# Kernel tuning notes

Measured on AMD Instinct MI355X. Metric: run time of the kernel, lower is better.

The kernel has to match this reference:

```python
import math
import jax, jax.numpy as jnp
import numpy as np

EPS = 1e-5  # BatchNorm2d default eps


def setup_inputs() -> dict:
    key = jax.random.key(0)
    ks = jax.random.split(key, 12)
    C, I = 256, 128  # in_channels, inter_channels (= C // reduction)
    n, h, w = 4, 64, 64
    s = 0.02
    return {
        "x": jax.random.normal(ks[0], (n, C, h, w), jnp.float32),
        "g_w": jax.random.normal(ks[1], (I, C), jnp.float32) * s,
        "g_b": jax.random.normal(ks[2], (I,), jnp.float32) * s,
        "theta_w": jax.random.normal(ks[3], (I, C), jnp.float32) * s,
        "theta_b": jax.random.normal(ks[4], (I,), jnp.float32) * s,
        "phi_w": jax.random.normal(ks[5], (I, C), jnp.float32) * s,
        "phi_b": jax.random.normal(ks[6], (I,), jnp.float32) * s,
        "out_w": jax.random.normal(ks[7], (C, I), jnp.float32) * s,
        "bn_gamma": jax.random.uniform(ks[8], (C,), jnp.float32, 0.5, 1.5),
        "bn_beta": jax.random.normal(ks[9], (C,), jnp.float32) * s,
        "bn_mean": jax.random.normal(ks[10], (C,), jnp.float32) * s,
        "bn_var": jax.random.uniform(ks[11], (C,), jnp.float32, 0.5, 1.5),
    }


def reference(x, g_w, g_b, theta_w, theta_b, phi_w, phi_b, out_w,
              bn_gamma, bn_beta, bn_mean, bn_var):
    n, c, h, w = x.shape
    xf = x.reshape(n, c, h * w)  # (n, C, N)

    def proj(Wm, b):  # 1x1 conv == per-position linear: (n, I, N)
        return jnp.einsum('ic,ncp->nip', Wm, xf) + b[None, :, None]

    g_x = proj(g_w, g_b)          # (n, I, N)
    theta_x = proj(theta_w, theta_b)  # (n, I, N)
    phi_x = proj(phi_w, phi_b)        # (n, I, N)

    # dot_product mode: softmax FIRST, then divide by sqrt(C) (faithful to source)
    scores = jnp.einsum('nip,niq->npq', theta_x, phi_x)  # (n, N, N)
    attn = jax.nn.softmax(scores, axis=-1) / math.sqrt(c)

    y = jnp.einsum('npq,niq->nip', attn, g_x)  # (n, I, N)
    y = y.reshape(n, -1, h, w)                 # (n, I, h, w)

    # conv_out: 1x1 conv (no bias) + BatchNorm2d (eval-mode running stats)
    y = jnp.einsum('oi,nihw->nohw', out_w, y)  # (n, C, h, w)
    inv = bn_gamma / jnp.sqrt(bn_var + EPS)
    y = y * inv[None, :, None, None] + (bn_beta - bn_mean * inv)[None, :, None, None]
    return y + x
```

## Files before the change

kernel.cpp:

```cpp
#include <hip/hip_runtime.h>

typedef short short8 __attribute__((ext_vector_type(8)));
typedef short short4v __attribute__((ext_vector_type(4)));
typedef float f32x4 __attribute__((ext_vector_type(4)));
typedef float f32x16 __attribute__((ext_vector_type(16)));
typedef unsigned int uint4v __attribute__((ext_vector_type(4)));
typedef unsigned int uint2v __attribute__((ext_vector_type(2)));

#define NB 4
#define CD 256
#define ID 128
#define NP 4096

static __device__ __forceinline__ short f2bf(float f){
  unsigned u = __float_as_uint(f);
  u += 0x7FFF + ((u >> 16) & 1);
  return (short)(u >> 16);
}
static __device__ __forceinline__ float bf2f(short s){
  unsigned u = ((unsigned)(unsigned short)s) << 16;
  return __uint_as_float(u);
}
static __device__ __forceinline__ unsigned cvtpk(float lo, float hi){
  unsigned r;
  asm("v_cvt_pk_bf16_f32 %0, %1, %2" : "=v"(r) : "v"(lo), "v"(hi));
  return r;
}
static __device__ __forceinline__ float fexp2(float x){
  float r;
  asm("v_exp_f32 %0, %1" : "=v"(r) : "v"(x));
  return r;
}
static __device__ __forceinline__ unsigned pack4_fp8(float a, float b, float c, float d){
  unsigned lo, hi;
  asm("v_cvt_pk_fp8_f32 %0, %1, %2" : "=v"(lo) : "v"(a), "v"(b));
  asm("v_cvt_pk_fp8_f32 %0, %1, %2" : "=v"(hi) : "v"(c), "v"(d));
  return (lo & 0xffffu) | (hi << 16);
}
static __device__ __forceinline__ unsigned char f2fp8(float v){
  unsigned u;
  asm("v_cvt_pk_fp8_f32 %0, %1, %1" : "=v"(u) : "v"(v));
  return (unsigned char)u;
}

static __device__ __forceinline__ void gload16(const void* g, void* l){
  __builtin_amdgcn_global_load_lds(
      (const __attribute__((address_space(1))) unsigned int*)g,
      (__attribute__((address_space(3))) unsigned int*)l, 16, 0, 0);
}

__global__ __launch_bounds__(256) void k_cvtw(const float* __restrict__ g_w,
    const float* __restrict__ th_w, const float* __restrict__ ph_w,
    const float* __restrict__ out_w, short* __restrict__ wb){
  int idx = (blockIdx.x * 256 + threadIdx.x) * 4;
  const float* s;
  int sel = idx >> 15;
  if(sel == 0) s = g_w; else if(sel == 1) s = th_w; else if(sel == 2) s = ph_w; else s = out_w;
  int off = idx & 32767;
  float4 v = *reinterpret_cast<const float4*>(s + off);
  short4v o = { f2bf(v.x), f2bf(v.y), f2bf(v.z), f2bf(v.w) };
  *reinterpret_cast<short4v*>(wb + idx) = o;
}

__global__ __launch_bounds__(512) void k_proj(const float* __restrict__ x,
    const short* __restrict__ wb, const float* __restrict__ g_b,
    const float* __restrict__ th_b, const float* __restrict__ ph_b,
    unsigned char* __restrict__ q8, unsigned char* __restrict__ k8,
    unsigned char* __restrict__ v8){
  __shared__ __align__(16) char smem[98304];
  char* XT = smem + 65536;
  int b = blockIdx.x;
  int n = b >> 6, pt = b & 63;
  int pb0 = pt * 64;
  int t = threadIdx.x, w = t >> 6, l = t & 63;
  int lr = l & 15, lg = l >> 4;
  int i0 = w * 16;

  const char* xg = (const char*)(x + ((size_t)n * CD) * NP + pb0);
#pragma unroll
  for(int i_ = 0; i_ < 8; ++i_){
    int dd = t * 16 + i_ * 8192;
    gload16(xg + (size_t)(dd >> 8) * 16384 + (dd & 255), smem + dd);
  }

  const short* gww = wb;
  const short* thw = wb + 32768;
  const short* phw = wb + 65536;
  short8 Wt[8], Wp[8], Wg[8];
#pragma unroll
  for(int kk = 0; kk < 8; ++kk){
    size_t wo = (size_t)(i0 + lr) * CD + kk * 32 + lg * 8;
    Wt[kk] = *reinterpret_cast<const short8*>(thw + wo);
    Wp[kk] = *reinterpret_cast<const short8*>(phw + wo);
    Wg[kk] = *reinterpret_cast<const short8*>(gww + wo);
  }
  float bt = th_b[i0 + lr];
  float bp = ph_b[i0 + lr];
  int ik = i0 + lr;
  int ip = (ik & 7) | (((ik >> 4) & 1) << 3) | (((ik >> 3) & 1) << 4) | ((ik >> 5) << 5);
  float gb[4];
#pragma unroll
  for(int r = 0; r < 4; ++r) gb[r] = g_b[i0 + lg * 4 + r];

  __syncthreads();

  {
    int p = l;
    const float* src = (const float*)smem;
    int key = (p & 15) << 4;
#pragma unroll
    for(int jj = 0; jj < 4; ++jj){
      unsigned pk4v[4];
#pragma unroll
      for(int q = 0; q < 4; ++q){
        int cp2 = w * 16 + jj * 4 + q;
        float f0 = src[(2 * cp2) * 64 + p];
        float f1 = src[(2 * cp2 + 1) * 64 + p];
        pk4v[q] = cvtpk(f0, f1);
      }
      uint4v v4 = { pk4v[0], pk4v[1], pk4v[2], pk4v[3] };
      *reinterpret_cast<uint4v*>(XT + p * 512 + ((w * 64 + jj * 16) ^ key)) = v4;
    }
  }
  __syncthreads();

  size_t vbase = ((size_t)n * 64 + pt) * 8192;
#pragma unroll
  for(int psub = 0; psub < 4; ++psub){
    int prow = psub * 16 + lr;
    short8 X[8];
#pragma unroll
    for(int kk = 0; kk < 8; ++kk)
      X[kk] = *reinterpret_cast<const short8*>(
          XT + prow * 512 + ((kk * 64 + lg * 16) ^ ((prow & 15) << 4)));
    f32x4 aT = {0.f,0.f,0.f,0.f}, aP = {0.f,0.f,0.f,0.f}, aG = {0.f,0.f,0.f,0.f};
#pragma unroll
    for(int kk = 0; kk < 8; ++kk){
      aT = __builtin_amdgcn_mfma_f32_16x16x32_bf16(X[kk], Wt[kk], aT, 0, 0, 0);
      aP = __builtin_amdgcn_mfma_f32_16x16x32_bf16(X[kk], Wp[kk], aP, 0, 0, 0);
      aG = __builtin_amdgcn_mfma_f32_16x16x32_bf16(Wg[kk], X[kk], aG, 0, 0, 0);
    }
#pragma unroll
    for(int r = 0; r < 4; ++r){
      size_t row = (size_t)(n * NP + pb0 + psub * 16 + lg * 4 + r);
      q8[row * ID + i0 + lr] = f2fp8((aT[r] + bt) * 1.44269504f);
      k8[row * ID + ip]      = f2fp8(aP[r] + bp);
    }
#pragma unroll
    for(int r = 0; r < 4; ++r){
      int ii = i0 + lg * 4 + r;
      v8[vbase + (psub >> 1) * 4096 + ((lr >> 3) & 1) * 2048 + ii * 16
               + (psub & 1) * 8 + (lr & 7)] = f2fp8(aG[r] + gb[r]);
    }
  }
}

__global__ __launch_bounds__(256, 2) void k_attn(const unsigned char* __restrict__ q8,
    const unsigned char* __restrict__ k8, const unsigned char* __restrict__ v8,
    short* __restrict__ po, float* __restrict__ psums){
  __shared__ __align__(16) char smem[65536];
  int b = blockIdx.x;
  int xcd = b & 7;
  int n = xcd >> 1;
  int kq = ((xcd & 1) << 1) | ((b >> 3) & 1);
  int qtl = b >> 4;
  int t = threadIdx.x, w = t >> 6, l = t & 63;
  int q31 = l & 31, hi = l >> 5;
  int pbase = qtl * 128 + w * 32;

  const char* kpanel = (const char*)k8 + ((size_t)(n * NP + kq * 1024)) * ID;
  const char* vpanel = (const char*)v8 + ((size_t)n * 64 + kq * 16) * 8192;
  const char* qbase  = (const char*)q8 + ((size_t)(n * NP + pbase)) * ID;

  uint2v Qf[8];
#pragma unroll
  for(int cst = 0; cst < 8; ++cst)
    Qf[cst] = *reinterpret_cast<const uint2v*>(qbase + q31 * 128 + cst * 16 + hi * 8);

  f32x16 Of[4];
#pragma unroll
  for(int db = 0; db < 4; ++db)
#pragma unroll
    for(int r = 0; r < 16; ++r) Of[db][r] = 0.f;
  float ps = 0.f;

#define STAGE(cb, kt_) do { \
    const char* kg_ = kpanel + (size_t)(kt_) * 8192; \
    const char* vg_ = vpanel + (size_t)(kt_) * 8192; \
    char* kld_ = smem + (cb) * 8192; \
    char* vld_ = smem + 16384 + (cb) * 8192; \
    _Pragma("unroll") \
    for(int i_ = 0; i_ < 2; ++i_){ \
      int dd = t * 16 + i_ * 4096; \
      int ks = (((dd >> 4) & 63) << 7) | ((dd >> 11) << 5) | (((dd >> 10) & 1) << 4); \
      gload16(kg_ + ks, kld_ + dd); \
      gload16(vg_ + dd, vld_ + dd); \
    } \
  } while(0)

  STAGE(0, 0);
  __syncthreads();

#pragma unroll 2
  for(int kt = 0; kt < 16; ++kt){
    const int pb = kt & 1;
    if(kt + 1 < 16) STAGE(pb ^ 1, kt + 1);
    const char* Kc = smem + pb * 8192;
    const char* Vc = smem + 16384 + pb * 8192;

    f32x16 Sa0, Sb0, Sa1, Sb1;
#pragma unroll
    for(int r = 0; r < 16; ++r){ Sa0[r] = 0.f; Sb0[r] = 0.f; Sa1[r] = 0.f; Sb1[r] = 0.f; }
    __builtin_amdgcn_s_setprio(1);
#pragma unroll
    for(int cp = 0; cp < 4; ++cp){
      uint4v Kp0 = *reinterpret_cast<const uint4v*>(
          Kc + cp * 2048 + hi * 1024 + q31 * 16);
      uint4v Kp1 = *reinterpret_cast<const uint4v*>(
          Kc + cp * 2048 + hi * 1024 + (32 + q31) * 16);
      uint2v Ka0 = { Kp0[0], Kp0[1] }, Kb0 = { Kp0[2], Kp0[3] };
      uint2v Ka1 = { Kp1[0], Kp1[1] }, Kb1 = { Kp1[2], Kp1[3] };
      long Qlo = __builtin_bit_cast(long, Qf[2*cp]);
      long Qhi = __builtin_bit_cast(long, Qf[2*cp+1]);
      Sa0 = __builtin_amdgcn_mfma_f32_32x32x16_fp8_fp8(__builtin_bit_cast(long, Ka0), Qlo, Sa0, 0, 0, 0);
      Sa1 = __builtin_amdgcn_mfma_f32_32x32x16_fp8_fp8(__builtin_bit_cast(long, Ka1), Qlo, Sa1, 0, 0, 0);
      Sb0 = __builtin_amdgcn_mfma_f32_32x32x16_fp8_fp8(__builtin_bit_cast(long, Kb0), Qhi, Sb0, 0, 0, 0);
      Sb1 = __builtin_amdgcn_mfma_f32_32x32x16_fp8_fp8(__builtin_bit_cast(long, Kb1), Qhi, Sb1, 0, 0, 0);
    }
    __builtin_amdgcn_s_setprio(0);

    long P00, P01;
    {
      float e[16];
#pragma unroll
      for(int r = 0; r < 16; ++r) e[r] = fexp2(Sa0[r] + Sb0[r] - 4.0f);
#pragma unroll
      for(int r = 0; r < 16; ++r) ps += e[r];
      unsigned u0 = pack4_fp8(e[0],  e[1],  e[2],  e[3]);
      unsigned u1 = pack4_fp8(e[4],  e[5],  e[6],  e[7]);
      unsigned u2 = pack4_fp8(e[8],  e[9],  e[10], e[11]);
      unsigned u3 = pack4_fp8(e[12], e[13], e[14], e[15]);
      asm("v_permlane32_swap_b32 %0, %1" : "+v"(u0), "+v"(u1));
      asm("v_permlane32_swap_b32 %0, %1" : "+v"(u2), "+v"(u3));
      P00 = __builtin_bit_cast(long, uint2v{u0, u1});
      P01 = __builtin_bit_cast(long, uint2v{u2, u3});
    }

    __builtin_amdgcn_s_setprio(1);
#pragma unroll
    for(int db = 0; db < 4; ++db){
      int d = db * 32 + q31;
      uint4v Vp = *reinterpret_cast<const uint4v*>(Vc + hi * 2048 + d * 16);
      uint2v Va = { Vp[0], Vp[1] }, Vb = { Vp[2], Vp[3] };
      Of[db] = __builtin_amdgcn_mfma_f32_32x32x16_fp8_fp8(P00, __builtin_bit_cast(long, Va), Of[db], 0, 0, 0);
      Of[db] = __builtin_amdgcn_mfma_f32_32x32x16_fp8_fp8(P01, __builtin_bit_cast(long, Vb), Of[db], 0, 0, 0);
    }
    __builtin_amdgcn_s_setprio(0);

    long P10, P11;
    {
      float e[16];
#pragma unroll
      for(int r = 0; r < 16; ++r) e[r] = fexp2(Sa1[r] + Sb1[r] - 4.0f);
#pragma unroll
      for(int r = 0; r < 16; ++r) ps += e[r];
      unsigned u0 = pack4_fp8(e[0],  e[1],  e[2],  e[3]);
      unsigned u1 = pack4_fp8(e[4],  e[5],  e[6],  e[7]);
      unsigned u2 = pack4_fp8(e[8],  e[9],  e[10], e[11]);
      unsigned u3 = pack4_fp8(e[12], e[13], e[14], e[15]);
      asm("v_permlane32_swap_b32 %0, %1" : "+v"(u0), "+v"(u1));
      asm("v_permlane32_swap_b32 %0, %1" : "+v"(u2), "+v"(u3));
      P10 = __builtin_bit_cast(long, uint2v{u0, u1});
      P11 = __builtin_bit_cast(long, uint2v{u2, u3});
    }

    __builtin_amdgcn_s_setprio(1);
#pragma unroll
    for(int db = 0; db < 4; ++db){
      int d = db * 32 + q31;
      uint4v Vp = *reinterpret_cast<const uint4v*>(Vc + 4096 + hi * 2048 + d * 16);
      uint2v Va = { Vp[0], Vp[1] }, Vb = { Vp[2], Vp[3] };
      Of[db] = __builtin_amdgcn_mfma_f32_32x32x16_fp8_fp8(P10, __builtin_bit_cast(long, Va), Of[db], 0, 0, 0);
      Of[db] = __builtin_amdgcn_mfma_f32_32x32x16_fp8_fp8(P11, __builtin_bit_cast(long, Vb), Of[db], 0, 0, 0);
    }
    __builtin_amdgcn_s_setprio(0);

    __syncthreads();
  }
#undef STAGE

  float pst = ps + __shfl_xor(ps, 32);
  if(hi == 0)
    psums[(size_t)kq * 16384 + n * NP + pbase + q31] = pst;

  float* ow = (float*)(smem + w * 16384);
#pragma unroll
  for(int reg = 0; reg < 16; ++reg){
    int q = (reg & 3) + 8 * (reg >> 2) + 4 * hi;
#pragma unroll
    for(int db = 0; db < 4; ++db)
      ow[q * 128 + db * 32 + q31] = Of[db][reg];
  }
  asm volatile("s_waitcnt lgkmcnt(0)" ::: "memory");
  __builtin_amdgcn_sched_barrier(0);
  short* pr = po + ((size_t)kq * 16384 + n * NP + pbase) * ID;
#pragma unroll
  for(int it = 0; it < 8; ++it){
    int o = it * 1024 + l * 16;
    int q = o >> 8, d0 = (o & 255) >> 1;
    f32x4 va = *reinterpret_cast<const f32x4*>(ow + q * 128 + d0);
    f32x4 vb = *reinterpret_cast<const f32x4*>(ow + q * 128 + d0 + 4);
    uint4v pk4 = { cvtpk(va[0], va[1]), cvtpk(va[2], va[3]),
                   cvtpk(vb[0], vb[1]), cvtpk(vb[2], vb[3]) };
    *reinterpret_cast<short8*>(pr + (size_t)q * ID + d0) = __builtin_bit_cast(short8, pk4);
  }
}

__global__ __launch_bounds__(512) void k_outproj(const short* __restrict__ po,
    const float* __restrict__ psums, const short* __restrict__ ow_b,
    const float* __restrict__ bng, const float* __restrict__ bnb,
    const float* __restrict__ bnm, const float* __restrict__ bnv,
    const float* __restrict__ x, float* __restrict__ out){
  __shared__ __align__(16) short XW[64 * 128];
  int b = blockIdx.x;
  int n = b >> 6, pt = b & 63;
  int pg0 = pt * 64;
  int t = threadIdx.x, w = t >> 6, l = t & 63;
  int lr = l & 15, lg = l >> 4;

  {
    int p = t >> 3, i0 = (t & 7) * 16;
    size_t qg = (size_t)n * NP + pg0 + p;
    float den = psums[qg] + psums[16384 + qg] + psums[32768 + qg] + psums[49152 + qg];
    float inv = 1.f / (16.f * den);
    const short* pp = po + qg * ID + i0;
    int key = (p & 15) << 4;
#pragma unroll
    for(int h = 0; h < 2; ++h){
      short8 b0 = *reinterpret_cast<const short8*>(pp + h * 8);
      short8 b1 = *reinterpret_cast<const short8*>(pp + (size_t)16384 * ID + h * 8);
      short8 b2 = *reinterpret_cast<const short8*>(pp + (size_t)32768 * ID + h * 8);
      short8 b3 = *reinterpret_cast<const short8*>(pp + (size_t)49152 * ID + h * 8);
      float f[8];
#pragma unroll
      for(int j = 0; j < 8; ++j)
        f[j] = (bf2f(b0[j]) + bf2f(b1[j]) + bf2f(b2[j]) + bf2f(b3[j])) * inv;
      uint4v pkv = { cvtpk(f[0], f[1]), cvtpk(f[2], f[3]),
                     cvtpk(f[4], f[5]), cvtpk(f[6], f[7]) };
      *reinterpret_cast<short8*>((char*)XW + p * 256 + ((i0 * 2 + h * 16) ^ key)) =
          __builtin_bit_cast(short8, pkv);
    }
  }
  __syncthreads();

  int c0 = w * 32;
  f32x4 acc[2][4];
#pragma unroll
  for(int mf = 0; mf < 2; ++mf)
#pragma unroll
    for(int nf = 0; nf < 4; ++nf) acc[mf][nf] = {0.f,0.f,0.f,0.f};
#pragma unroll
  for(int kk = 0; kk < 4; ++kk){
    short8 Af[2];
#pragma unroll
    for(int mf = 0; mf < 2; ++mf)
      Af[mf] = *reinterpret_cast<const short8*>(ow_b + (size_t)(c0 + mf * 16 + lr) * ID + kk * 32 + lg * 8);
#pragma unroll
    for(int nf = 0; nf < 4; ++nf){
      int prow = nf * 16 + lr;
      short8 Bf = *reinterpret_cast<const short8*>(
          (char*)XW + prow * 256 + ((kk * 64 + lg * 16) ^ ((prow & 15) << 4)));
#pragma unroll
      for(int mf = 0; mf < 2; ++mf)
        acc[mf][nf] = __builtin_amdgcn_mfma_f32_16x16x32_bf16(Af[mf], Bf, acc[mf][nf], 0, 0, 0);
    }
  }

#pragma unroll
  for(int mf = 0; mf < 2; ++mf){
    int cb = c0 + mf * 16 + lg * 4;
    float inv[4], sh[4];
#pragma unroll
    for(int r = 0; r < 4; ++r){
      float iv = bng[cb + r] * rsqrtf(bnv[cb + r] + 1e-5f);
      inv[r] = iv;
      sh[r] = bnb[cb + r] - bnm[cb + r] * iv;
    }
#pragma unroll
    for(int nf = 0; nf < 4; ++nf){
      int p = pg0 + nf * 16 + lr;
#pragma unroll
      for(int r = 0; r < 4; ++r){
        size_t idx = ((size_t)(n * CD + cb + r)) * NP + p;
        out[idx] = acc[mf][nf][r] * inv[r] + sh[r] + x[idx];
      }
    }
  }
}

extern "C" void kernel_launch(void* const* d_in, const int* in_sizes, int n_in,
                              void* d_out, int out_size, void* d_ws, size_t ws_size,
                              hipStream_t stream){
  const float* x    = (const float*)d_in[0];
  const float* g_w  = (const float*)d_in[1];
  const float* g_b  = (const float*)d_in[2];
  const float* th_w = (const float*)d_in[3];
  const float* th_b = (const float*)d_in[4];
  const float* ph_w = (const float*)d_in[5];
  const float* ph_b = (const float*)d_in[6];
  const float* out_w= (const float*)d_in[7];
  const float* bng  = (const float*)d_in[8];
  const float* bnb  = (const float*)d_in[9];
  const float* bnm  = (const float*)d_in[10];
  const float* bnv  = (const float*)d_in[11];
  float* out = (float*)d_out;
  char* ws = (char*)d_ws;

  unsigned char* q8  = (unsigned char*)(ws + (size_t)(8u  << 20));
  unsigned char* k8  = (unsigned char*)(ws + (size_t)(12u << 20));
  unsigned char* v8  = (unsigned char*)(ws + (size_t)(16u << 20));
  short* wb          = (short*)(ws + (size_t)(24u << 20));
  short* po          = (short*)(ws + (size_t)(25u << 20));
  float* psum        = (float*)(ws + (size_t)(41u << 20));

  k_cvtw<<<128, 256, 0, stream>>>(g_w, th_w, ph_w, out_w, wb);
  k_proj<<<256, 512, 0, stream>>>(x, wb, g_b, th_b, ph_b, q8, k8, v8);
  k_attn<<<512, 256, 0, stream>>>(q8, k8, v8, po, psum);
  k_outproj<<<256, 512, 0, stream>>>(po, psum, wb + 98304, bng, bnb, bnm, bnv, x, out);
}
```

Baseline: 64.24 us.

## Fold weight bf16 conversion into consumers and triple-buffer attention K/V staging

Removes the separate weight-conversion kernel: the projection and output-projection kernels now load fp32 weights and pack them to bf16 in registers, saving one launch and a workspace round trip. The attention kernel moves from double to triple buffering of the K/V tiles, prefetching two tiles ahead. It waits with explicit vmcnt counts and a single barrier per iteration instead of two __syncthreads. In exchange the kernel uses more LDS and depends on precise waitcnt accounting, and each block re-reads the fp32 weights (twice the bytes).

```diff
diff --git a/kernel.cpp b/kernel.cpp
--- a/kernel.cpp
+++ b/kernel.cpp
@@ -1,7 +1,6 @@
 #include <hip/hip_runtime.h>
 
 typedef short short8 __attribute__((ext_vector_type(8)));
-typedef short short4v __attribute__((ext_vector_type(4)));
 typedef float f32x4 __attribute__((ext_vector_type(4)));
 typedef float f32x16 __attribute__((ext_vector_type(16)));
 typedef unsigned int uint4v __attribute__((ext_vector_type(4)));
@@ -12,11 +11,6 @@
 #define ID 128
 #define NP 4096
 
-static __device__ __forceinline__ short f2bf(float f){
-  unsigned u = __float_as_uint(f);
-  u += 0x7FFF + ((u >> 16) & 1);
-  return (short)(u >> 16);
-}
 static __device__ __forceinline__ float bf2f(short s){
   unsigned u = ((unsigned)(unsigned short)s) << 16;
   return __uint_as_float(u);
@@ -42,6 +36,12 @@
   asm("v_cvt_pk_fp8_f32 %0, %1, %1" : "=v"(u) : "v"(v));
   return (unsigned char)u;
 }
+static __device__ __forceinline__ short8 wfrag(const float* p){
+  float4 a = *reinterpret_cast<const float4*>(p);
+  float4 b = *reinterpret_cast<const float4*>(p + 4);
+  uint4v u = { cvtpk(a.x, a.y), cvtpk(a.z, a.w), cvtpk(b.x, b.y), cvtpk(b.z, b.w) };
+  return __builtin_bit_cast(short8, u);
+}
 
 static __device__ __forceinline__ void gload16(const void* g, void* l){
   __builtin_amdgcn_global_load_lds(
@@ -49,21 +49,9 @@
       (__attribute__((address_space(3))) unsigned int*)l, 16, 0, 0);
 }
 
-__global__ __launch_bounds__(256) void k_cvtw(const float* __restrict__ g_w,
-    const float* __restrict__ th_w, const float* __restrict__ ph_w,
-    const float* __restrict__ out_w, short* __restrict__ wb){
-  int idx = (blockIdx.x * 256 + threadIdx.x) * 4;
-  const float* s;
-  int sel = idx >> 15;
-  if(sel == 0) s = g_w; else if(sel == 1) s = th_w; else if(sel == 2) s = ph_w; else s = out_w;
-  int off = idx & 32767;
-  float4 v = *reinterpret_cast<const float4*>(s + off);
-  short4v o = { f2bf(v.x), f2bf(v.y), f2bf(v.z), f2bf(v.w) };
-  *reinterpret_cast<short4v*>(wb + idx) = o;
-}
-
 __global__ __launch_bounds__(512) void k_proj(const float* __restrict__ x,
-    const short* __restrict__ wb, const float* __restrict__ g_b,
+    const float* __restrict__ g_w, const float* __restrict__ th_w,
+    const float* __restrict__ ph_w, const float* __restrict__ g_b,
     const float* __restrict__ th_b, const float* __restrict__ ph_b,
     unsigned char* __restrict__ q8, unsigned char* __restrict__ k8,
     unsigned char* __restrict__ v8){
@@ -83,16 +71,13 @@
     gload16(xg + (size_t)(dd >> 8) * 16384 + (dd & 255), smem + dd);
   }
 
-  const short* gww = wb;
-  const short* thw = wb + 32768;
-  const short* phw = wb + 65536;
   short8 Wt[8], Wp[8], Wg[8];
 #pragma unroll
   for(int kk = 0; kk < 8; ++kk){
     size_t wo = (size_t)(i0 + lr) * CD + kk * 32 + lg * 8;
-    Wt[kk] = *reinterpret_cast<const short8*>(thw + wo);
-    Wp[kk] = *reinterpret_cast<const short8*>(phw + wo);
-    Wg[kk] = *reinterpret_cast<const short8*>(gww + wo);
+    Wt[kk] = wfrag(th_w + wo);
+    Wp[kk] = wfrag(ph_w + wo);
+    Wg[kk] = wfrag(g_w + wo);
   }
   float bt = th_b[i0 + lr];
   float bp = ph_b[i0 + lr];
@@ -188,7 +173,7 @@
     const char* kg_ = kpanel + (size_t)(kt_) * 8192; \
     const char* vg_ = vpanel + (size_t)(kt_) * 8192; \
     char* kld_ = smem + (cb) * 8192; \
-    char* vld_ = smem + 16384 + (cb) * 8192; \
+    char* vld_ = smem + 24576 + (cb) * 8192; \
     _Pragma("unroll") \
     for(int i_ = 0; i_ < 2; ++i_){ \
       int dd = t * 16 + i_ * 4096; \
@@ -199,14 +184,17 @@
   } while(0)
 
   STAGE(0, 0);
-  __syncthreads();
-
-#pragma unroll 2
+  STAGE(1, 1);
+
   for(int kt = 0; kt < 16; ++kt){
-    const int pb = kt & 1;
-    if(kt + 1 < 16) STAGE(pb ^ 1, kt + 1);
-    const char* Kc = smem + pb * 8192;
-    const char* Vc = smem + 16384 + pb * 8192;
+    if(kt < 15) asm volatile("s_waitcnt vmcnt(4)" ::: "memory");
+    else        asm volatile("s_waitcnt vmcnt(0)" ::: "memory");
+    __builtin_amdgcn_s_barrier();
+    __builtin_amdgcn_sched_barrier(0);
+    if(kt + 2 < 16) STAGE((kt + 2) % 3, kt + 2);
+    int cb = kt % 3;
+    const char* Kc = smem + cb * 8192;
+    const char* Vc = smem + 24576 + cb * 8192;
 
     f32x16 Sa0, Sb0, Sa1, Sb1;
 #pragma unroll
@@ -284,10 +272,12 @@
       Of[db] = __builtin_amdgcn_mfma_f32_32x32x16_fp8_fp8(P11, __builtin_bit_cast(long, Vb), Of[db], 0, 0, 0);
     }
     __builtin_amdgcn_s_setprio(0);
-
-    __syncthreads();
   }
 #undef STAGE
+
+  asm volatile("s_waitcnt vmcnt(0)" ::: "memory");
+  __builtin_amdgcn_s_barrier();
+  __builtin_amdgcn_sched_barrier(0);
 
   float pst = ps + __shfl_xor(ps, 32);
   if(hi == 0)
@@ -317,7 +307,7 @@
 }
 
 __global__ __launch_bounds__(512) void k_outproj(const short* __restrict__ po,
-    const float* __restrict__ psums, const short* __restrict__ ow_b,
+    const float* __restrict__ psums, const float* __restrict__ out_w,
     const float* __restrict__ bng, const float* __restrict__ bnb,
     const float* __restrict__ bnm, const float* __restrict__ bnv,
     const float* __restrict__ x, float* __restrict__ out){
@@ -351,9 +341,22 @@
           __builtin_bit_cast(short8, pkv);
     }
   }
+
+  int c0 = w * 32;
+  short8 Af[4][2];
+#pragma unroll
+  for(int kk = 0; kk < 4; ++kk)
+#pragma unroll
+    for(int mf = 0; mf < 2; ++mf){
+      float4 a = *reinterpret_cast<const float4*>(
+          out_w + (size_t)(c0 + mf * 16 + lr) * ID + kk * 32 + lg * 8);
+      float4 bb = *reinterpret_cast<const float4*>(
+          out_w + (size_t)(c0 + mf * 16 + lr) * ID + kk * 32 + lg * 8 + 4);
+      uint4v u = { cvtpk(a.x, a.y), cvtpk(a.z, a.w), cvtpk(bb.x, bb.y), cvtpk(bb.z, bb.w) };
+      Af[kk][mf] = __builtin_bit_cast(short8, u);
+    }
   __syncthreads();
 
-  int c0 = w * 32;
   f32x4 acc[2][4];
 #pragma unroll
   for(int mf = 0; mf < 2; ++mf)
@@ -361,10 +364,6 @@
     for(int nf = 0; nf < 4; ++nf) acc[mf][nf] = {0.f,0.f,0.f,0.f};
 #pragma unroll
   for(int kk = 0; kk < 4; ++kk){
-    short8 Af[2];
-#pragma unroll
-    for(int mf = 0; mf < 2; ++mf)
-      Af[mf] = *reinterpret_cast<const short8*>(ow_b + (size_t)(c0 + mf * 16 + lr) * ID + kk * 32 + lg * 8);
 #pragma unroll
     for(int nf = 0; nf < 4; ++nf){
       int prow = nf * 16 + lr;
@@ -372,7 +371,7 @@
           (char*)XW + prow * 256 + ((kk * 64 + lg * 16) ^ ((prow & 15) << 4)));
 #pragma unroll
       for(int mf = 0; mf < 2; ++mf)
-        acc[mf][nf] = __builtin_amdgcn_mfma_f32_16x16x32_bf16(Af[mf], Bf, acc[mf][nf], 0, 0, 0);
+        acc[mf][nf] = __builtin_amdgcn_mfma_f32_16x16x32_bf16(Af[kk][mf], Bf, acc[mf][nf], 0, 0, 0);
     }
   }
 
@@ -419,12 +418,10 @@
   unsigned char* q8  = (unsigned char*)(ws + (size_t)(8u  << 20));
   unsigned char* k8  = (unsigned char*)(ws + (size_t)(12u << 20));
   unsigned char* v8  = (unsigned char*)(ws + (size_t)(16u << 20));
-  short* wb          = (short*)(ws + (size_t)(24u << 20));
   short* po          = (short*)(ws + (size_t)(25u << 20));
   float* psum        = (float*)(ws + (size_t)(41u << 20));
 
-  k_cvtw<<<128, 256, 0, stream>>>(g_w, th_w, ph_w, out_w, wb);
-  k_proj<<<256, 512, 0, stream>>>(x, wb, g_b, th_b, ph_b, q8, k8, v8);
+  k_proj<<<256, 512, 0, stream>>>(x, g_w, th_w, ph_w, g_b, th_b, ph_b, q8, k8, v8);
   k_attn<<<512, 256, 0, stream>>>(q8, k8, v8, po, psum);
-  k_outproj<<<256, 512, 0, stream>>>(po, psum, wb + 98304, bng, bnb, bnm, bnv, x, out);
-}
+  k_outproj<<<256, 512, 0, stream>>>(po, psum, out_w, bng, bnb, bnm, bnv, x, out);
+}
```

Measured after the change: 67.43 us. +5.0%, slower.
